# Performance work log

Measured on AMD Instinct MI355X. Metric: run time of the kernel, lower is better.

The kernel has to match this reference:

```python
import jax, jax.numpy as jnp
import numpy as np

# GPT-2 small structural constants (hardcoded in the original module)
L, H, D, DH, F, V, P, S, NC = 12, 12, 768, 64, 3072, 50257, 1024, 128, 29

def _ln(x, g, b, eps=1e-5):
    m = x.mean(-1, keepdims=True)
    v = ((x - m) ** 2).mean(-1, keepdims=True)
    return (x - m) * jax.lax.rsqrt(v + eps) * g + b

def _split_w(W):  # [D, D] -> [H, D, DH]: torch _split_heads on the last (output) dim
    return jnp.transpose(W.reshape(D, H, DH), (1, 0, 2))

def _attn_heads(xln, Wqh, Wkh, Wvh, Woh, qb, kb, vb, mask):
    # xln: [H, S, D] per-head circuit inputs. Computes the weight-product attention
    # branch: (xln@Wq+bq)(xln@Wk+bk)^T scores (algebraically identical to the four
    # W_mhqk bias-expanded terms in the source), causal softmax, then
    # attn @ ((xln@Wv+bv) @ W_mho) which equals attn@Output_mhov + attn@bv_Wo.
    q = jnp.einsum('hse,hed->hsd', xln, Wqh) + qb[:, None, :]
    k = jnp.einsum('hse,hed->hsd', xln, Wkh) + kb[:, None, :]
    v = jnp.einsum('hse,hed->hsd', xln, Wvh) + vb[:, None, :]
    s = jnp.einsum('hsd,htd->hst', q, k) / (DH ** 0.5)
    s = jnp.where(mask, s, jnp.finfo(s.dtype).min)
    a = jax.nn.softmax(s, axis=-1)
    ctx = jnp.einsum('hst,htd->hsd', a, v)
    return jnp.einsum('hsd,hdf->hsf', ctx, Woh)  # [H, S, D]

def _check1(x, r, records):
    # check_representation: subtract refined-matrix-gated recorded circuit tensors
    # from layers 0..i-1 (rows >= i of records are still zero, so full contraction
    # equals contracting records[0:i+1]).
    return x - jnp.einsum('lc,lcsd->sd', r, records)

def _checkH(x, rh, records):  # batched over the 12 per-head checks
    return x[None] - jnp.einsum('hlc,lcsd->hsd', rh, records)

def _forward(input_ids, refined_matrix, wte, wpe, qkv_w, qkv_b, proj_w, proj_b,
             ln1_g, ln1_b, ln2_g, ln2_b, fc_w, fc_b, mproj_w, mproj_b, lnf_g, lnf_b):
    rm = refined_matrix.astype(wte.dtype)                 # [L*NC, L, NC]
    h = wte[input_ids[0]] + wpe[:S]                       # [S, D]
    records = jnp.zeros((L, NC, S, D), dtype=h.dtype)     # record_circuit_tensor_all
    mask = jnp.tril(jnp.ones((S, S), dtype=bool))
    gelu = lambda x: jax.nn.gelu(x, approximate=True)     # GPT-2 gelu_new
    for i in range(L):
        Wq, Wk, Wv = jnp.split(qkv_w[i], 3, axis=1)
        Wqh, Wkh, Wvh = _split_w(Wq), _split_w(Wk), _split_w(Wv)
        qb = qkv_b[i][:D].reshape(H, DH)
        kb = qkv_b[i][D:2 * D].reshape(H, DH)
        vb = qkv_b[i][2 * D:].reshape(H, DH)
        Woh = proj_w[i].reshape(H, DH, D)                 # W_mho per head
        base = i * NC
        if i > 0:
            c1 = _check1(h, rm[base], records)                       # check 0
            x2 = _checkH(h, rm[base + 1:base + 1 + H], records)      # checks 1..12
            x3 = _check1(h, rm[base + 13], records)                  # check 13
            x4 = _checkH(h, rm[base + 14:base + 14 + H], records)    # checks 14..25
        else:
            c1, x3 = h, h
            x2 = jnp.broadcast_to(h, (H, S, D))
            x4 = x2
        # circuit 2: per-head attention via weight products
        x2ln = _ln(x2, ln1_g[i], ln1_b[i])
        head2 = _attn_heads(x2ln, Wqh, Wkh, Wvh, Woh, qb, kb, vb, mask)
        c2 = head2.sum(0)
        residual = c1 + c2 + proj_b[i]                    # + W_obias
        # full MLP stream on the residual (with c_fc bias, no c_proj bias)
        stream = gelu(_ln(residual, ln2_g[i], ln2_b[i]) @ fc_w[i] + fc_b[i]) @ mproj_w[i]
        # circuit 3: bias-free MLP of the (double-LN'd) checked layer input
        x3ln = _ln(_ln(x3, ln1_g[i], ln1_b[i]), ln2_g[i], ln2_b[i])
        c3 = gelu(x3ln @ fc_w[i]) @ mproj_w[i]
        # circuit 4: per-head attention branch -> MLP composition
        x4ln = _ln(x4, ln1_g[i], ln1_b[i])
        head4 = _attn_heads(x4ln, Wqh, Wkh, Wvh, Woh, qb, kb, vb, mask)
        c4_heads = gelu(_ln(head4, ln2_g[i], ln2_b[i]) @ fc_w[i]) @ mproj_w[i]
        c5 = stream - c3 - c4_heads.sum(0)                # nonlinearity compensation
        c6 = jnp.broadcast_to(mproj_b[i], (S, D))
        ob = jnp.broadcast_to(proj_b[i], (S, D))
        rec = jnp.concatenate([c1[None], head2, c3[None], c4_heads,
                               c5[None], c6[None], ob[None]], axis=0)  # [29, S, D]
        records = records.at[i].set(rec)
        h = residual + stream + mproj_b[i]
    return _ln(h, lnf_g, lnf_b) @ wte.T                   # logits [S, V]

def setup_inputs():
    key = jax.random.key(0)
    ks = jax.random.split(key, 16)
    sd = 0.02
    n = lambda k, shp: (jax.random.normal(k, shp) * sd).astype(jnp.float32)
    return {
        'input_ids': jax.random.randint(ks[0], (1, S), 0, V),
        'label_ids': jax.random.randint(ks[1], (1, S), 0, V),
        'refined_matrix': jax.random.randint(ks[2], (L * NC, L, NC), 0, 2).astype(jnp.int32),
        'wte': n(ks[3], (V, D)),
        'wpe': n(ks[4], (P, D)),
        'qkv_w': n(ks[5], (L, D, 3 * D)),
        'qkv_b': n(ks[6], (L, 3 * D)),
        'proj_w': n(ks[7], (L, D, D)),
        'proj_b': n(ks[8], (L, D)),
        'ln1_g': jnp.ones((L, D), jnp.float32),
        'ln1_b': jnp.zeros((L, D), jnp.float32),
        'ln2_g': jnp.ones((L, D), jnp.float32),
        'ln2_b': jnp.zeros((L, D), jnp.float32),
        'fc_w': n(ks[9], (L, D, F)),
        'fc_b': n(ks[10], (L, F)),
        'mproj_w': n(ks[11], (L, F, D)),
        'mproj_b': n(ks[12], (L, D)),
        'lnf_g': jnp.ones((D,), jnp.float32),
        'lnf_b': jnp.zeros((D,), jnp.float32),
    }

def reference(input_ids, label_ids, refined_matrix, wte, wpe, qkv_w, qkv_b, proj_w, proj_b,
              ln1_g, ln1_b, ln2_g, ln2_b, fc_w, fc_b, mproj_w, mproj_b, lnf_g, lnf_b):
    return _forward(input_ids, refined_matrix, wte, wpe, qkv_w, qkv_b, proj_w, proj_b,
                    ln1_g, ln1_b, ln2_g, ln2_b, fc_w, fc_b, mproj_w, mproj_b, lnf_g, lnf_b)
```

## Files before the change

kernel.cpp:

```cpp
#include <hip/hip_runtime.h>

#define SS 128
#define DD 768
#define HH 12
#define DHD 64
#define FF 3072
#define VV 50257
#define NCC 29
#define NCR 27
#define LL 12
#define SD (SS*DD)
#define SF (SS*FF)
#define TMAX (LL*NCC)
#define TRMAX (LL*NCR)

typedef unsigned short u16;
typedef __attribute__((ext_vector_type(8))) short short8;
typedef __attribute__((ext_vector_type(4))) float f32x4;

__device__ inline u16 f2bf(float f) {
    union { float f; unsigned u; } x; x.f = f;
    unsigned r = x.u + 0x7fffu + ((x.u >> 16) & 1u);
    return (u16)(r >> 16);
}

__global__ void k_masku(const int* __restrict__ rm, unsigned* __restrict__ lmu) {
    int idx = blockIdx.x * 256 + threadIdx.x;
    if (idx >= LL * TRMAX) return;
    int i = idx / TRMAX, t = idx % TRMAX;
    int l = t / NCR, c = t % NCR;
    unsigned m = 0;
    for (int j = 0; j < 26; j++)
        m |= (unsigned)(rm[(size_t)(i * NCC + j) * TMAX + l * NCC + c] & 1) << j;
    lmu[idx] = m;
}

__global__ void k_bias(const int* __restrict__ rm, const float* __restrict__ proj_b,
                       const float* __restrict__ mproj_b, float* __restrict__ bc) {
    int idx = blockIdx.x * 256 + threadIdx.x;
    if (idx >= LL * 26 * DD) return;
    int i = idx / (26 * DD);
    int r = idx % (26 * DD);
    int j = r / DD, d = r % DD;
    float s = 0.f;
    for (int l = 0; l < i; l++) {
        const int* row = rm + (size_t)(i * NCC + j) * TMAX + l * NCC;
        s += (float)(row[27] & 1) * mproj_b[(size_t)l * DD + d];
        s += (float)(row[28] & 1) * proj_b[(size_t)l * DD + d];
    }
    bc[idx] = s;
}

__global__ void k_embed(const int* __restrict__ ids, const float* __restrict__ wte,
                        const float* __restrict__ wpe, float* __restrict__ h) {
    int sd = blockIdx.x * 256 + threadIdx.x;
    if (sd >= SD) return;
    int s = sd / DD, d = sd % DD;
    h[sd] = wte[(size_t)ids[s] * DD + d] + wpe[sd];
}

__global__ void k_cvt(const float* __restrict__ in, u16* __restrict__ out, int n4) {
    int i = blockIdx.x * 256 + threadIdx.x;
    if (i >= n4) return;
    float4 v = *(const float4*)(in + (size_t)i * 4);
    u16* o = out + (size_t)i * 4;
    o[0] = f2bf(v.x); o[1] = f2bf(v.y); o[2] = f2bf(v.z); o[3] = f2bf(v.w);
}

__global__ void k_qkvb(const float* __restrict__ qkv_b, float* __restrict__ qkvbp) {
    int idx = blockIdx.x * 256 + threadIdx.x;
    if (idx >= LL * 3 * DD) return;
    int l = idx / (3 * DD), r = idx % (3 * DD);
    int p = r / DD, rem = r % DD, h = rem / DHD, j = rem % DHD;
    qkvbp[(size_t)l * 3 * DD + h * 192 + p * DHD + j] = qkv_b[idx];
}

__global__ __launch_bounds__(256) void k_wt(const float* __restrict__ W, u16* __restrict__ WT,
                                            int K, int N, int remap,
                                            long long sW, long long sWT) {
    __shared__ float T[64][65];
    const float* Wb = W + (size_t)blockIdx.z * sW;
    u16* WTb = WT + (size_t)blockIdx.z * sWT;
    int n0 = blockIdx.x * 64, k0 = blockIdx.y * 64;
    int c = threadIdx.x & 63, r0 = threadIdx.x >> 6;
#pragma unroll
    for (int i = 0; i < 16; i++) {
        int r = r0 + 4 * i;
        T[r][c] = Wb[(size_t)(k0 + r) * N + n0 + c];
    }
    __syncthreads();
    int ob = n0 >> 6;
    if (remap) { int p = ob / 12, h = ob % 12; ob = h * 3 + p; }
    size_t orow0 = (size_t)ob * 64;
#pragma unroll
    for (int i = 0; i < 16; i++) {
        int a = r0 + 4 * i;
        WTb[(orow0 + a) * K + k0 + c] = f2bf(T[c][a]);
    }
}

__global__ __launch_bounds__(256) void k_check(
    const float* __restrict__ records, const unsigned* __restrict__ lmu,
    const float* __restrict__ bc,
    const float* __restrict__ h, float* __restrict__ rec0, float* __restrict__ x24,
    float* __restrict__ x3, int layer) {
    __shared__ float red[4][13][128];
    int lane = threadIdx.x & 63, w = threadIdx.x >> 6;
    int sd0 = blockIdx.x * 128;
    int d0 = sd0 % DD;
    int sd = sd0 + lane * 2;
    int T = layer * NCR;
    int Tq = (T + 3) >> 2;
    int tb = w * Tq, te = tb + Tq; if (te > T) te = T;
    float2 acc[26];
#pragma unroll
    for (int j = 0; j < 26; j++) { acc[j].x = 0.f; acc[j].y = 0.f; }
    const unsigned* lm = lmu + layer * TRMAX;
    const float* rp = records + sd;
    int t = tb;
    for (; t + 8 <= te; t += 8) {
        float2 r[8];
        unsigned mv[8];
#pragma unroll
        for (int u = 0; u < 8; u++) r[u] = *(const float2*)(rp + (size_t)(t + u) * SD);
#pragma unroll
        for (int u = 0; u < 8; u++) mv[u] = lm[t + u];
#pragma unroll
        for (int u = 0; u < 8; u++) {
            unsigned m = __builtin_amdgcn_readfirstlane(mv[u]);
#pragma unroll
            for (int j = 0; j < 26; j++) {
                float mm = (m & (1u << j)) ? 1.0f : 0.0f;
                acc[j].x = fmaf(mm, r[u].x, acc[j].x);
                acc[j].y = fmaf(mm, r[u].y, acc[j].y);
            }
        }
    }
    for (; t < te; t++) {
        float2 r = *(const float2*)(rp + (size_t)t * SD);
        unsigned m = __builtin_amdgcn_readfirstlane(lm[t]);
#pragma unroll
        for (int j = 0; j < 26; j++) {
            float mm = (m & (1u << j)) ? 1.0f : 0.0f;
            acc[j].x = fmaf(mm, r.x, acc[j].x);
            acc[j].y = fmaf(mm, r.y, acc[j].y);
        }
    }
    const float* bcl = bc + (size_t)layer * 26 * DD;
#pragma unroll
    for (int pass = 0; pass < 2; pass++) {
        int jb = pass * 13;
#pragma unroll
        for (int j2 = 0; j2 < 13; j2++)
            *(float2*)&red[w][j2][lane * 2] = acc[jb + j2];
        __syncthreads();
        for (int o = threadIdx.x; o < 13 * 128; o += 256) {
            int j2 = o >> 7, sdl = o & 127;
            int j = jb + j2;
            float s = red[0][j2][sdl] + red[1][j2][sdl] + red[2][j2][sdl] + red[3][j2][sdl];
            float v = h[sd0 + sdl] - s - bcl[(size_t)j * DD + d0 + sdl];
            float* dst;
            if (j == 0) dst = rec0;
            else if (j <= 12) dst = x24 + (size_t)(j - 1) * SD;
            else if (j == 13) dst = x3;
            else dst = x24 + (size_t)(12 + j - 14) * SD;
            dst[sd0 + sdl] = v;
        }
        __syncthreads();
    }
}

__device__ inline void wave_ln(float (&vals)[12], int lane, const float* __restrict__ g,
                               const float* __restrict__ b) {
    float s = 0.f;
#pragma unroll
    for (int i = 0; i < 12; i++) s += vals[i];
#pragma unroll
    for (int m = 32; m >= 1; m >>= 1) s += __shfl_xor(s, m, 64);
    float mean = s * (1.f / DD);
    float vs = 0.f;
#pragma unroll
    for (int i = 0; i < 12; i++) { float d = vals[i] - mean; vs += d * d; }
#pragma unroll
    for (int m = 32; m >= 1; m >>= 1) vs += __shfl_xor(vs, m, 64);
    float rstd = rsqrtf(vs * (1.f / DD) + 1e-5f);
#pragma unroll
    for (int i = 0; i < 12; i++)
        vals[i] = (vals[i] - mean) * rstd * g[lane + 64 * i] + b[lane + 64 * i];
}

__global__ __launch_bounds__(256) void k_ln(const float* __restrict__ in, float* __restrict__ outf,
                                            u16* __restrict__ outb,
                                            const float* __restrict__ g, const float* __restrict__ b,
                                            int R) {
    int row = blockIdx.x * 4 + (threadIdx.x >> 6);
    if (row >= R) return;
    int lane = threadIdx.x & 63;
    const float* x = in + (size_t)row * DD;
    float vals[12];
#pragma unroll
    for (int i = 0; i < 12; i++) vals[i] = x[lane + 64 * i];
    wave_ln(vals, lane, g, b);
#pragma unroll
    for (int i = 0; i < 12; i++) {
        int d = lane + 64 * i;
        if (outf) outf[(size_t)row * DD + d] = vals[i];
        if (outb) outb[(size_t)row * DD + d] = f2bf(vals[i]);
    }
}

__global__ __launch_bounds__(256) void k_rln(const float* __restrict__ reci,
                                             const float* __restrict__ x3,
                                             const float* __restrict__ tmp4,
                                             const float* __restrict__ proj_b_i,
                                             float* __restrict__ resid,
                                             u16* __restrict__ mlpAb,
                                             const float* __restrict__ l1g, const float* __restrict__ l1b,
                                             const float* __restrict__ l2g, const float* __restrict__ l2b) {
    int rowid = blockIdx.x * 4 + (threadIdx.x >> 6);
    int z = rowid >> 7, s = rowid & 127;
    int lane = threadIdx.x & 63;
    float vals[12];
    if (z == 0) {
        const float* src = x3 + (size_t)s * DD;
#pragma unroll
        for (int i = 0; i < 12; i++) vals[i] = src[lane + 64 * i];
        wave_ln(vals, lane, l1g, l1b);
    } else if (z <= 12) {
        const float* src = tmp4 + (size_t)(z - 1) * SD + (size_t)s * DD;
#pragma unroll
        for (int i = 0; i < 12; i++) vals[i] = src[lane + 64 * i];
    } else {
        const float* base = reci + (size_t)s * DD;
#pragma unroll
        for (int i = 0; i < 12; i++) {
            int d = lane + 64 * i;
            float a = base[d];
#pragma unroll
            for (int j = 1; j <= 12; j++) a += base[(size_t)j * SD + d];
            a += proj_b_i[d];
            vals[i] = a;
            resid[(size_t)s * DD + d] = a;
        }
    }
    wave_ln(vals, lane, l2g, l2b);
    u16* o = mlpAb + (size_t)z * SD + (size_t)s * DD;
#pragma unroll
    for (int i = 0; i < 12; i++) o[lane + 64 * i] = f2bf(vals[i]);
}

__global__ __launch_bounds__(256) void k_mm(
    const u16* __restrict__ A, const u16* __restrict__ BT,
    const float* __restrict__ bias, void* __restrict__ Cv, void* __restrict__ Cv2,
    int N, int K, int lda, int ldbt, int ldc,
    long long sA, long long sBT, long long sC, long long sBias,
    int zMod, int zHi, int biasLo, int mode) {
    __shared__ u16 As[128][40];
    __shared__ u16 Bs[64][40];
    int z = blockIdx.z;
    int zb = z % zMod;
    const u16* Ab = A + (size_t)z * sA;
    const u16* Bb = BT + (size_t)zb * sBT;
    int n0 = blockIdx.x * 64;
    int nSplit = gridDim.y;
    int kLen = K / nSplit;
    int kOff = blockIdx.y * kLen;
    int kEnd = kOff + kLen;
    int tid = threadIdx.x;
    int lane = tid & 63, wid = tid >> 6;
    int wm = (wid >> 1) * 64, wn = (wid & 1) * 32;
    int l15 = lane & 15, l4 = lane >> 4;
    int sr = tid >> 2, sseg = tid & 3;
    int bn = n0 + sr;
    f32x4 acc[4][2];
#pragma unroll
    for (int i = 0; i < 4; i++) { acc[i][0] = (f32x4)0.f; acc[i][1] = (f32x4)0.f; }
    uint4 zero; zero.x = 0u; zero.y = 0u; zero.z = 0u; zero.w = 0u;
    uint4 a0 = *(const uint4*)(Ab + (size_t)sr * lda + kOff + sseg * 8);
    uint4 a1 = *(const uint4*)(Ab + (size_t)(sr + 64) * lda + kOff + sseg * 8);
    uint4 bv = (bn < N) ? *(const uint4*)(Bb + (size_t)bn * ldbt + kOff + sseg * 8) : zero;
    for (int k0 = kOff; k0 < kEnd; k0 += 32) {
        __syncthreads();
        *(uint4*)&As[sr][sseg * 8] = a0;
        *(uint4*)&As[sr + 64][sseg * 8] = a1;
        *(uint4*)&Bs[sr][sseg * 8] = bv;
        __syncthreads();
        if (k0 + 32 < kEnd) {
            a0 = *(const uint4*)(Ab + (size_t)sr * lda + k0 + 32 + sseg * 8);
            a1 = *(const uint4*)(Ab + (size_t)(sr + 64) * lda + k0 + 32 + sseg * 8);
            bv = (bn < N) ? *(const uint4*)(Bb + (size_t)bn * ldbt + k0 + 32 + sseg * 8) : zero;
        }
        short8 af[4], bfr[2];
#pragma unroll
        for (int i = 0; i < 4; i++) af[i] = *(const short8*)&As[wm + i * 16 + l15][l4 * 8];
#pragma unroll
        for (int j = 0; j < 2; j++) bfr[j] = *(const short8*)&Bs[wn + j * 16 + l15][l4 * 8];
#pragma unroll
        for (int i = 0; i < 4; i++)
#pragma unroll
            for (int j = 0; j < 2; j++)
                acc[i][j] = __builtin_amdgcn_mfma_f32_16x16x32_bf16(af[i], bfr[j], acc[i][j], 0, 0, 0);
    }
    const float* bp = (bias != nullptr && z >= biasLo) ? bias + (size_t)zb * sBias : nullptr;
    void* Cuse;
    int zc;
    if (nSplit > 1) { Cuse = Cv; zc = z * nSplit + blockIdx.y; }
    else { Cuse = (z >= zHi) ? Cv2 : Cv; zc = (z >= zHi) ? z - zHi : z; }
    if (mode == 0) {
        float* Cb = (float*)Cuse + (size_t)zc * sC;
#pragma unroll
        for (int i = 0; i < 4; i++) {
            int row = wm + i * 16 + l4 * 4;
#pragma unroll
            for (int j = 0; j < 2; j++) {
                int col = n0 + wn + j * 16 + l15;
                if (col >= N) continue;
                float bb = bp ? bp[col] : 0.f;
#pragma unroll
                for (int r = 0; r < 4; r++)
                    Cb[(size_t)(row + r) * ldc + col] = acc[i][j][r] + bb;
            }
        }
    } else {
        u16* Cb = (u16*)Cuse + (size_t)zc * sC;
#pragma unroll
        for (int i = 0; i < 4; i++) {
            int row = wm + i * 16 + l4 * 4;
#pragma unroll
            for (int j = 0; j < 2; j++) {
                int col = n0 + wn + j * 16 + l15;
                if (col >= N) continue;
                float bb = bp ? bp[col] : 0.f;
#pragma unroll
                for (int r = 0; r < 4; r++) {
                    float v = acc[i][j][r] + bb;
                    float c = v + 0.044715f * v * v * v;
                    float gv = 0.5f * v * (1.f + tanhf(0.7978845608028654f * c));
                    Cb[(size_t)(row + r) * ldc + col] = f2bf(gv);
                }
            }
        }
    }
}

__global__ __launch_bounds__(256) void k_attnp(const float* __restrict__ qkvp,
                                               const float* __restrict__ qbias,
                                               const u16* __restrict__ projT,
                                               float* __restrict__ outLo,
                                               float* __restrict__ outHi) {
    __shared__ float kv[SS * DHD];
    __shared__ float qs[16][DHD];
    __shared__ float sc[16][130];
    __shared__ u16 cxs[16][72];
    int z = blockIdx.y, s0 = blockIdx.x * 16;
    int hb = z % 12;
    const float* p0 = qkvp + (size_t)z * 4 * (SS * 192);
    const float* p1 = p0 + SS * 192;
    const float* p2 = p1 + SS * 192;
    const float* p3 = p2 + SS * 192;
    const float* qb = qbias + (size_t)hb * 192;
    int tid = threadIdx.x;
    for (int idx = tid; idx < SS * DHD; idx += 256) {
        int t = idx >> 6, d = idx & 63;
        int o = t * 192 + 64 + d;
        kv[idx] = p0[o] + p1[o] + p2[o] + p3[o] + qb[64 + d];
    }
    for (int idx = tid; idx < 16 * DHD; idx += 256) {
        int r = idx >> 6, d = idx & 63;
        int o = (s0 + r) * 192 + d;
        qs[r][d] = p0[o] + p1[o] + p2[o] + p3[o] + qb[d];
    }
    __syncthreads();
    int r = tid >> 4, tt = tid & 15;
    int s = s0 + r;
    float pl[8];
#pragma unroll
    for (int u = 0; u < 8; u++) {
        int t = tt + 16 * u;
        float dot;
        if (t <= s) {
            dot = 0.f;
            for (int d = 0; d < DHD; d++) dot += qs[r][d] * kv[t * DHD + d];
            dot *= 0.125f;
        } else {
            dot = -1e30f;
        }
        pl[u] = dot;
    }
    float mx = pl[0];
#pragma unroll
    for (int u = 1; u < 8; u++) mx = fmaxf(mx, pl[u]);
#pragma unroll
    for (int m = 1; m < 16; m <<= 1) mx = fmaxf(mx, __shfl_xor(mx, m, 16));
    float sum = 0.f;
#pragma unroll
    for (int u = 0; u < 8; u++) { pl[u] = __expf(pl[u] - mx); sum += pl[u]; }
#pragma unroll
    for (int m = 1; m < 16; m <<= 1) sum += __shfl_xor(sum, m, 16);
    float inv = 1.f / sum;
#pragma unroll
    for (int u = 0; u < 8; u++) sc[r][tt + 16 * u] = pl[u] * inv;
    __syncthreads();
    for (int idx = tid; idx < SS * DHD; idx += 256) {
        int t = idx >> 6, d = idx & 63;
        int o = t * 192 + 128 + d;
        kv[idx] = p0[o] + p1[o] + p2[o] + p3[o] + qb[128 + d];
    }
    __syncthreads();
    int d = tid & 63, r0 = tid >> 6;
#pragma unroll
    for (int u = 0; u < 4; u++) {
        int rr = r0 + 4 * u;
        float a = 0.f;
        for (int t = 0; t < SS; t++) a += sc[rr][t] * kv[t * DHD + d];
        cxs[rr][d] = f2bf(a);
    }
    __syncthreads();
    int lane = tid & 63, w = tid >> 6;
    int l15 = lane & 15, l4 = lane >> 4;
    short8 af[2];
#pragma unroll
    for (int ks = 0; ks < 2; ks++) af[ks] = *(const short8*)&cxs[l15][ks * 32 + l4 * 8];
    float* ob = (z < 12) ? outLo + (size_t)z * SD : outHi + (size_t)(z - 12) * SD;
#pragma unroll
    for (int nt = 0; nt < 12; nt++) {
        int n0t = (w * 12 + nt) * 16;
        f32x4 acc = (f32x4)0.f;
#pragma unroll
        for (int ks = 0; ks < 2; ks++) {
            short8 bf = *(const short8*)(projT + (size_t)(n0t + l15) * DD + hb * DHD + ks * 32 + l4 * 8);
            acc = __builtin_amdgcn_mfma_f32_16x16x32_bf16(af[ks], bf, acc, 0, 0, 0);
        }
#pragma unroll
        for (int rr = 0; rr < 4; rr++)
            ob[(size_t)(s0 + l4 * 4 + rr) * DD + n0t + l15] = acc[rr];
    }
}

__global__ void k_red(const float* __restrict__ part, const float* __restrict__ resid,
                      const float* __restrict__ mproj_b_i,
                      float* __restrict__ reci, float* __restrict__ h) {
    int sd = blockIdx.x * 256 + threadIdx.x;
    if (sd >= SD) return;
    int d = sd % DD;
    float v0 = 0.f, s4 = 0.f, st = 0.f;
#pragma unroll
    for (int zz = 0; zz < 14; zz++) {
        const float* p = part + (size_t)zz * 4 * SD + sd;
        float v = p[0] + p[SD] + p[2 * SD] + p[3 * SD];
        if (zz == 0) { v0 = v; reci[(size_t)13 * SD + sd] = v; }
        else if (zz <= 12) { s4 += v; reci[(size_t)(13 + zz) * SD + sd] = v; }
        else st = v;
    }
    reci[(size_t)26 * SD + sd] = st - v0 - s4;
    h[sd] = resid[sd] + st + mproj_b_i[d];
}

extern "C" void kernel_launch(void* const* d_in, const int* in_sizes, int n_in,
                              void* d_out, int out_size, void* d_ws, size_t ws_size,
                              hipStream_t stream) {
    const int* ids = (const int*)d_in[0];
    const int* rm = (const int*)d_in[2];
    const float* wte = (const float*)d_in[3];
    const float* wpe = (const float*)d_in[4];
    const float* qkv_w = (const float*)d_in[5];
    const float* qkv_b = (const float*)d_in[6];
    const float* proj_w = (const float*)d_in[7];
    const float* proj_b = (const float*)d_in[8];
    const float* ln1_g = (const float*)d_in[9];
    const float* ln1_b = (const float*)d_in[10];
    const float* ln2_g = (const float*)d_in[11];
    const float* ln2_b = (const float*)d_in[12];
    const float* fc_w = (const float*)d_in[13];
    const float* fc_b = (const float*)d_in[14];
    const float* mproj_w = (const float*)d_in[15];
    const float* mproj_b = (const float*)d_in[16];
    const float* lnf_g = (const float*)d_in[17];
    const float* lnf_b = (const float*)d_in[18];
    float* out = (float*)d_out;

    float* ws = (float*)d_ws;
    size_t off = 0;
    float* records = ws + off; off += (size_t)LL * NCR * SD;
    float* x24  = ws + off; off += (size_t)24 * SD;
    float* tmp4 = ws + off; off += (size_t)12 * SD;
    float* h    = ws + off; off += SD;
    float* x3   = ws + off; off += SD;
    float* resid= ws + off; off += SD;
    float* qkvp = ws + off; off += (size_t)24 * 4 * SS * 192;
    float* mpp  = ws + off; off += (size_t)14 * 4 * SD;
    float* qkvbp= ws + off; off += (size_t)LL * 3 * DD;
    float* bc   = ws + off; off += (size_t)LL * 26 * DD;
    u16* xlnb  = (u16*)(ws + off); off += (size_t)24 * SD / 2;
    u16* mlpAb = (u16*)(ws + off); off += (size_t)14 * SD / 2;
    u16* hfcb  = (u16*)(ws + off); off += (size_t)14 * SF / 2;
    u16* lnfb  = (u16*)(ws + off); off += SD / 2;
    u16* qkvhT = (u16*)(ws + off); off += (size_t)LL * 2304 * DD / 2;
    u16* fcT   = (u16*)(ws + off); off += (size_t)LL * FF * DD / 2;
    u16* mprojT= (u16*)(ws + off); off += (size_t)LL * DD * FF / 2;
    u16* projT = (u16*)(ws + off); off += (size_t)LL * DD * DD / 2;
    u16* wteb  = (u16*)(ws + off); off += (size_t)VV * DD / 2;
    unsigned* lmu = (unsigned*)(ws + off);

    k_masku<<<(LL * TRMAX + 255) / 256, 256, 0, stream>>>(rm, lmu);
    k_bias<<<(LL * 26 * DD + 255) / 256, 256, 0, stream>>>(rm, proj_b, mproj_b, bc);
    k_embed<<<SD / 256, 256, 0, stream>>>(ids, wte, wpe, h);
    k_cvt<<<((VV * DD / 4) + 255) / 256, 256, 0, stream>>>(wte, wteb, VV * DD / 4);
    k_qkvb<<<(LL * 3 * DD + 255) / 256, 256, 0, stream>>>(qkv_b, qkvbp);
    k_wt<<<dim3(36, 12, 12), 256, 0, stream>>>(qkv_w, qkvhT, DD, 3 * DD, 1,
                                               (long long)DD * 3 * DD, (long long)2304 * DD);
    k_wt<<<dim3(48, 12, 12), 256, 0, stream>>>(fc_w, fcT, DD, FF, 0,
                                               (long long)DD * FF, (long long)FF * DD);
    k_wt<<<dim3(12, 48, 12), 256, 0, stream>>>(mproj_w, mprojT, FF, DD, 0,
                                               (long long)FF * DD, (long long)DD * FF);
    k_wt<<<dim3(12, 12, 12), 256, 0, stream>>>(proj_w, projT, DD, DD, 0,
                                               (long long)DD * DD, (long long)DD * DD);

    for (int i = 0; i < LL; i++) {
        float* reci = records + (size_t)i * NCR * SD;
        const float* l1g = ln1_g + i * DD; const float* l1b = ln1_b + i * DD;
        const float* l2g = ln2_g + i * DD; const float* l2b = ln2_b + i * DD;
        const u16* qkvhTi = qkvhT + (size_t)i * 2304 * DD;
        const u16* fcTi = fcT + (size_t)i * FF * DD;
        const u16* mprojTi = mprojT + (size_t)i * DD * FF;
        const u16* projTi = projT + (size_t)i * DD * DD;

        k_check<<<SD / 128, 256, 0, stream>>>(records, lmu, bc, h, reci, x24, x3, i);

        k_ln<<<24 * SS / 4, 256, 0, stream>>>(x24, nullptr, xlnb, l1g, l1b, 24 * SS);
        k_mm<<<dim3(3, 4, 24), 256, 0, stream>>>(
            xlnb, qkvhTi, nullptr, qkvp, nullptr,
            192, DD, DD, DD, 192, SD, (long long)192 * DD, (long long)SS * 192, 0, 12, 9999, 99, 0);
        k_attnp<<<dim3(SS / 16, 24), 256, 0, stream>>>(qkvp, qkvbp + (size_t)i * 3 * DD,
                                                       projTi, reci + SD, tmp4);
        k_rln<<<14 * SS / 4, 256, 0, stream>>>(reci, x3, tmp4, proj_b + i * DD, resid, mlpAb,
                                               l1g, l1b, l2g, l2b);
        k_mm<<<dim3(48, 1, 14), 256, 0, stream>>>(
            mlpAb, fcTi, fc_b + (size_t)i * FF, hfcb, nullptr,
            FF, DD, DD, DD, FF, SD, 0, SF, 0, 1, 9999, 13, 1);
        k_mm<<<dim3(12, 4, 14), 256, 0, stream>>>(
            hfcb, mprojTi, nullptr, mpp, nullptr,
            DD, FF, FF, FF, DD, SF, 0, SD, 0, 1, 9999, 99, 0);
        k_red<<<SD / 256, 256, 0, stream>>>(mpp, resid, mproj_b + i * DD, reci, h);
    }

    k_ln<<<SS / 4, 256, 0, stream>>>(h, nullptr, lnfb, lnf_g, lnf_b, SS);
    k_mm<<<dim3((VV + 63) / 64, 1, 1), 256, 0, stream>>>(
        lnfb, wteb, nullptr, out, nullptr,
        VV, DD, DD, DD, VV, 0, 0, 0, 0, 1, 9999, 99, 0);
}
```

Before: 1.820 ms.

## Fuse MLP partial reduction into next layer's check kernel

Folds the per-layer reduction of the MLP-projection partial sums (k_red) into the following layer's k_check. The fused kernel rebuilds h locally, writes the previous layer's records, and uses the 14 freshly reduced tensors straight from shared memory instead of re-reading them from global records. This removes one launch per layer and a global round-trip for those records. In exchange, wave 3 of k_check takes on extra serial FMA work, and a small k_hfin kernel is still needed after the final layer.

```diff
diff --git a/kernel.cpp b/kernel.cpp
--- a/kernel.cpp
+++ b/kernel.cpp
@@ -101,17 +101,49 @@
 
 __global__ __launch_bounds__(256) void k_check(
     const float* __restrict__ records, const unsigned* __restrict__ lmu,
-    const float* __restrict__ bc,
-    const float* __restrict__ h, float* __restrict__ rec0, float* __restrict__ x24,
-    float* __restrict__ x3, int layer) {
-    __shared__ float red[4][13][128];
+    const float* __restrict__ bc, const float* __restrict__ h0,
+    float* __restrict__ rec0, float* __restrict__ x24, float* __restrict__ x3,
+    int layer, const float* __restrict__ mpp, const float* __restrict__ resid,
+    const float* __restrict__ mproj_b_p, float* __restrict__ recprev) {
+    __shared__ float smem[4][13][128];
+    __shared__ float hloc[128];
+    float (*vred)[128] = (float(*)[128])&smem[0][0][0];
     int lane = threadIdx.x & 63, w = threadIdx.x >> 6;
     int sd0 = blockIdx.x * 128;
     int d0 = sd0 % DD;
     int sd = sd0 + lane * 2;
     int T = layer * NCR;
-    int Tq = (T + 3) >> 2;
-    int tb = w * Tq, te = tb + Tq; if (te > T) te = T;
+    int Tm = (layer > 0) ? T - 14 : 0;
+    if (layer > 0) {
+        for (int idx = threadIdx.x; idx < 14 * 128; idx += 256) {
+            int z = idx >> 7, sdl = idx & 127;
+            const float* p = mpp + (size_t)z * 4 * SD + sd0 + sdl;
+            vred[z][sdl] = p[0] + p[SD] + p[2 * SD] + p[3 * SD];
+        }
+        __syncthreads();
+        if (threadIdx.x < 128) {
+            int sdl = threadIdx.x;
+            int sdg = sd0 + sdl, d = d0 + sdl;
+            float v0 = vred[0][sdl];
+            float st = vred[13][sdl];
+            float s4 = 0.f;
+#pragma unroll
+            for (int z = 1; z <= 12; z++) s4 += vred[z][sdl];
+            float c5 = st - v0 - s4;
+            hloc[sdl] = resid[sdg] + st + mproj_b_p[d];
+            recprev[(size_t)13 * SD + sdg] = v0;
+#pragma unroll
+            for (int z = 1; z <= 12; z++) recprev[(size_t)(13 + z) * SD + sdg] = vred[z][sdl];
+            recprev[(size_t)26 * SD + sdg] = c5;
+            vred[13][sdl] = c5;
+        }
+        __syncthreads();
+    } else {
+        if (threadIdx.x < 128) hloc[threadIdx.x] = h0[sd0 + threadIdx.x];
+        __syncthreads();
+    }
+    int Tq = (Tm + 3) >> 2;
+    int tb = w * Tq, te = tb + Tq; if (te > Tm) te = Tm;
     float2 acc[26];
 #pragma unroll
     for (int j = 0; j < 26; j++) { acc[j].x = 0.f; acc[j].y = 0.f; }
@@ -146,19 +178,33 @@
             acc[j].y = fmaf(mm, r.y, acc[j].y);
         }
     }
+    if (layer > 0 && w == 3) {
+#pragma unroll
+        for (int c = 0; c < 14; c++) {
+            unsigned m = __builtin_amdgcn_readfirstlane(lm[Tm + c]);
+            float rx = vred[c][lane * 2], ry = vred[c][lane * 2 + 1];
+#pragma unroll
+            for (int j = 0; j < 26; j++) {
+                float mm = (m & (1u << j)) ? 1.0f : 0.0f;
+                acc[j].x = fmaf(mm, rx, acc[j].x);
+                acc[j].y = fmaf(mm, ry, acc[j].y);
+            }
+        }
+    }
+    __syncthreads();
     const float* bcl = bc + (size_t)layer * 26 * DD;
 #pragma unroll
     for (int pass = 0; pass < 2; pass++) {
         int jb = pass * 13;
 #pragma unroll
         for (int j2 = 0; j2 < 13; j2++)
-            *(float2*)&red[w][j2][lane * 2] = acc[jb + j2];
+            *(float2*)&smem[w][j2][lane * 2] = acc[jb + j2];
         __syncthreads();
         for (int o = threadIdx.x; o < 13 * 128; o += 256) {
             int j2 = o >> 7, sdl = o & 127;
             int j = jb + j2;
-            float s = red[0][j2][sdl] + red[1][j2][sdl] + red[2][j2][sdl] + red[3][j2][sdl];
-            float v = h[sd0 + sdl] - s - bcl[(size_t)j * DD + d0 + sdl];
+            float s = smem[0][j2][sdl] + smem[1][j2][sdl] + smem[2][j2][sdl] + smem[3][j2][sdl];
+            float v = hloc[sdl] - s - bcl[(size_t)j * DD + d0 + sdl];
             float* dst;
             if (j == 0) dst = rec0;
             else if (j <= 12) dst = x24 + (size_t)(j - 1) * SD;
@@ -437,22 +483,13 @@
     }
 }
 
-__global__ void k_red(const float* __restrict__ part, const float* __restrict__ resid,
-                      const float* __restrict__ mproj_b_i,
-                      float* __restrict__ reci, float* __restrict__ h) {
+__global__ void k_hfin(const float* __restrict__ mpp, const float* __restrict__ resid,
+                       const float* __restrict__ mproj_b_i, float* __restrict__ h) {
     int sd = blockIdx.x * 256 + threadIdx.x;
     if (sd >= SD) return;
     int d = sd % DD;
-    float v0 = 0.f, s4 = 0.f, st = 0.f;
-#pragma unroll
-    for (int zz = 0; zz < 14; zz++) {
-        const float* p = part + (size_t)zz * 4 * SD + sd;
-        float v = p[0] + p[SD] + p[2 * SD] + p[3 * SD];
-        if (zz == 0) { v0 = v; reci[(size_t)13 * SD + sd] = v; }
-        else if (zz <= 12) { s4 += v; reci[(size_t)(13 + zz) * SD + sd] = v; }
-        else st = v;
-    }
-    reci[(size_t)26 * SD + sd] = st - v0 - s4;
+    const float* p = mpp + (size_t)13 * 4 * SD + sd;
+    float st = p[0] + p[SD] + p[2 * SD] + p[3 * SD];
     h[sd] = resid[sd] + st + mproj_b_i[d];
 }
 
@@ -518,6 +555,8 @@
 
     for (int i = 0; i < LL; i++) {
         float* reci = records + (size_t)i * NCR * SD;
+        float* recprev = records + (size_t)(i > 0 ? i - 1 : 0) * NCR * SD;
+        const float* mbp = mproj_b + (size_t)(i > 0 ? i - 1 : 0) * DD;
         const float* l1g = ln1_g + i * DD; const float* l1b = ln1_b + i * DD;
         const float* l2g = ln2_g + i * DD; const float* l2b = ln2_b + i * DD;
         const u16* qkvhTi = qkvhT + (size_t)i * 2304 * DD;
@@ -525,7 +564,8 @@
         const u16* mprojTi = mprojT + (size_t)i * DD * FF;
         const u16* projTi = projT + (size_t)i * DD * DD;
 
-        k_check<<<SD / 128, 256, 0, stream>>>(records, lmu, bc, h, reci, x24, x3, i);
+        k_check<<<SD / 128, 256, 0, stream>>>(records, lmu, bc, h, reci, x24, x3, i,
+                                              mpp, resid, mbp, recprev);
 
         k_ln<<<24 * SS / 4, 256, 0, stream>>>(x24, nullptr, xlnb, l1g, l1b, 24 * SS);
         k_mm<<<dim3(3, 4, 24), 256, 0, stream>>>(
@@ -541,9 +581,9 @@
         k_mm<<<dim3(12, 4, 14), 256, 0, stream>>>(
             hfcb, mprojTi, nullptr, mpp, nullptr,
             DD, FF, FF, FF, DD, SF, 0, SD, 0, 1, 9999, 99, 0);
-        k_red<<<SD / 256, 256, 0, stream>>>(mpp, resid, mproj_b + i * DD, reci, h);
-    }
-
+    }
+
+    k_hfin<<<SD / 256, 256, 0, stream>>>(mpp, resid, mproj_b + (size_t)11 * DD, h);
     k_ln<<<SS / 4, 256, 0, stream>>>(h, nullptr, lnfb, lnf_g, lnf_b, SS);
     k_mm<<<dim3((VV + 63) / 64, 1, 1), 256, 0, stream>>>(
         lnfb, wteb, nullptr, out, nullptr,
```

Result: slower. 2.663 ms (+46.3%).
